# Optimization experiments

Measured on AMD Instinct MI355X. Metric: run time of the kernel, lower is better.

## Reference

```python
import jax, jax.numpy as jnp
import numpy as np

H = 2048          # hidden_size
HEAD = 64         # head_size
NH = H // HEAD    # n_heads = 32
B, T = 4, 4096
LORA_MIX = 32     # per-branch rank of time_maa low-rank mixer (5 branches)
LORA_DECAY = 64   # rank of decay low-rank mixer


def setup_inputs() -> dict:
    key = jax.random.key(0)
    ks = jax.random.split(key, 24)
    s = 0.02  # small init scale keeps tanh/silu in sane range
    inp = {
        "hidden": jax.random.normal(ks[0], (B, T, H), jnp.float32),
        "attn_x": jax.random.normal(ks[1], (B, H), jnp.float32),
        "attn_kv": jax.random.normal(ks[2], (B, NH, HEAD, HEAD), jnp.float32),
        "ffn_x": jax.random.normal(ks[3], (B, H), jnp.float32),
        "time_maa_x": jax.random.normal(ks[4], (1, 1, H), jnp.float32) * s,
        "time_maa_w": jax.random.normal(ks[5], (1, 1, H), jnp.float32) * s,
        "time_maa_k": jax.random.normal(ks[6], (1, 1, H), jnp.float32) * s,
        "time_maa_v": jax.random.normal(ks[7], (1, 1, H), jnp.float32) * s,
        "time_maa_r": jax.random.normal(ks[8], (1, 1, H), jnp.float32) * s,
        "time_maa_g": jax.random.normal(ks[9], (1, 1, H), jnp.float32) * s,
        "time_maa_w1": jax.random.normal(ks[10], (H, LORA_MIX * 5), jnp.float32) * s,
        "time_maa_w2": jax.random.normal(ks[11], (5, LORA_MIX, H), jnp.float32) * s,
        "time_decay": jax.random.normal(ks[12], (1, 1, H), jnp.float32) * s,
        "time_decay_w1": jax.random.normal(ks[13], (H, LORA_DECAY), jnp.float32) * s,
        "time_decay_w2": jax.random.normal(ks[14], (LORA_DECAY, H), jnp.float32) * s,
        "time_faaaa": jax.random.normal(ks[15], (NH, HEAD), jnp.float32) * s,
        "receptance_w": jax.random.normal(ks[16], (H, H), jnp.float32) * s,
        "key_w": jax.random.normal(ks[17], (H, H), jnp.float32) * s,
        "value_w": jax.random.normal(ks[18], (H, H), jnp.float32) * s,
        "gate_w": jax.random.normal(ks[19], (H, H), jnp.float32) * s,
        "output_w": jax.random.normal(ks[20], (H, H), jnp.float32) * s,
    }
    return inp


def reference(hidden, attn_x, attn_kv, ffn_x,
              time_maa_x, time_maa_w, time_maa_k, time_maa_v, time_maa_r, time_maa_g,
              time_maa_w1, time_maa_w2,
              time_decay, time_decay_w1, time_decay_w2, time_faaaa,
              receptance_w, key_w, value_w, gate_w, output_w):
    b, t, h = hidden.shape
    # token shift: prepend previous chunk's last token state
    shifted = jnp.concatenate([attn_x[:, None, :], hidden[:, :-1, :]], axis=1)  # [B,T,H]
    x = hidden
    xx = shifted - x
    # low-rank data-dependent mixing coefficients (5 branches)
    xxx = x + xx * time_maa_x                                        # [B,T,H]
    xxx = jnp.tanh(xxx.reshape(-1, h) @ time_maa_w1)                 # [B*T, 5*32]
    xxx = xxx.reshape(-1, 5, LORA_MIX).transpose(1, 0, 2)            # [5, B*T, 32]
    xxx = jnp.einsum('fnr,frh->fnh', xxx, time_maa_w2)               # [5, B*T, H]
    xxx = xxx.reshape(5, b, t, h)
    mw, mk, mv, mr, mg = xxx[0], xxx[1], xxx[2], xxx[3], xxx[4]
    # note: source uses additive mix (x + xx + coeff), faithful to code as written
    td_in = x + xx + (time_maa_w + mw)
    k_in = x + xx + (time_maa_k + mk)
    v_in = x + xx + (time_maa_v + mv)
    r_in = x + xx + (time_maa_r + mr)
    g_in = x + xx + (time_maa_g + mg)
    receptance = jnp.einsum('bth,hd->btd', r_in, receptance_w)
    key = jnp.einsum('bth,hd->btd', k_in, key_w)
    value = jnp.einsum('bth,hd->btd', v_in, value_w)
    gate = jax.nn.silu(jnp.einsum('bth,hd->btd', g_in, gate_w))
    td = jnp.tanh(jnp.einsum('bth,hr->btr', td_in, time_decay_w1))
    td = jnp.einsum('btr,rh->bth', td, time_decay_w2)
    td = time_decay + td                                              # [B,T,H] per-channel decay
    attn_x_new = hidden[:, -1]                                        # [B,H]
    return (receptance, key, value, gate, td, attn_x_new)
```

## Files before the change

kernel.cpp:

```cpp
#include <hip/hip_runtime.h>

#define H 2048
#define TT 4096
#define BB 4
#define NROWS (BB * TT)
#define NTH ((size_t)NROWS * H)
#define KCAT (H + 32)
#define KC8  (H + 64)
#define NTH64 ((size_t)NROWS * 64)

typedef __attribute__((ext_vector_type(8))) short bh8;
typedef __attribute__((ext_vector_type(4))) float f32x4;

__device__ inline unsigned short f2bf(float f) {
    union { float f; unsigned u; } v; v.f = f;
    unsigned r = v.u + 0x7fff + ((v.u >> 16) & 1);
    return (unsigned short)(r >> 16);
}
__device__ inline float bf2f(unsigned short u) {
    union { unsigned u; float f; } v; v.u = ((unsigned)u) << 16; return v.f;
}
__device__ inline void gload_lds16(const void* g, void* l) {
    __builtin_amdgcn_global_load_lds(
        (const __attribute__((address_space(1))) void*)g,
        (__attribute__((address_space(3))) void*)l, 16, 0, 0);
}

__global__ __launch_bounds__(256) void prep_kernel(
    const float* __restrict__ hidden, const float* __restrict__ attn_x,
    const float* __restrict__ tmx,
    unsigned short* __restrict__ shifted, unsigned short* __restrict__ xin) {
    size_t i = ((size_t)blockIdx.x * 256 + threadIdx.x) * 4;
    int n = (int)(i >> 11);
    int h = (int)(i & 2047);
    int t = n & (TT - 1);
    float4 x = *(const float4*)(hidden + i);
    float4 s;
    if (t == 0) {
        int b = n >> 12;
        s = *(const float4*)(attn_x + ((size_t)b << 11) + h);
    } else {
        s = *(const float4*)(hidden + (i - H));
    }
    float4 m = *(const float4*)(tmx + h);
    ushort4 sh, xi;
    sh.x = f2bf(s.x); sh.y = f2bf(s.y); sh.z = f2bf(s.z); sh.w = f2bf(s.w);
    xi.x = f2bf(x.x + (s.x - x.x) * m.x);
    xi.y = f2bf(x.y + (s.y - x.y) * m.y);
    xi.z = f2bf(x.z + (s.z - x.z) * m.z);
    xi.w = f2bf(x.w + (s.w - x.w) * m.w);
    *(ushort4*)(shifted + i) = sh;
    *(ushort4*)(xin + i) = xi;
}

__global__ __launch_bounds__(256) void transpose_kernel(
    const float* __restrict__ in, unsigned short* __restrict__ outp,
    int R, int C, int ldo) {
    __shared__ float tile[32][33];
    int tx = threadIdx.x & 31, ty = threadIdx.x >> 5;
    int r0 = blockIdx.y * 32, c0 = blockIdx.x * 32;
    for (int i = ty; i < 32; i += 8) {
        int r = r0 + i, c = c0 + tx;
        tile[i][tx] = (r < R && c < C) ? in[(size_t)r * C + c] : 0.f;
    }
    __syncthreads();
    for (int i = ty; i < 32; i += 8) {
        int c = c0 + i, r = r0 + tx;
        if (c < C && r < R) outp[(size_t)c * ldo + r] = f2bf(tile[tx][i]);
    }
}

__global__ __launch_bounds__(256) void transpose4_kernel(
    const float* __restrict__ w0, const float* __restrict__ w1,
    const float* __restrict__ w2, const float* __restrict__ w3,
    unsigned short* __restrict__ d0, unsigned short* __restrict__ d1,
    unsigned short* __restrict__ d2, unsigned short* __restrict__ d3) {
    __shared__ float tile[32][33];
    int bz = blockIdx.z;
    const float* in = bz == 0 ? w0 : bz == 1 ? w1 : bz == 2 ? w2 : w3;
    unsigned short* outp = bz == 0 ? d0 : bz == 1 ? d1 : bz == 2 ? d2 : d3;
    int tx = threadIdx.x & 31, ty = threadIdx.x >> 5;
    int r0 = blockIdx.y * 32, c0 = blockIdx.x * 32;
    for (int i = ty; i < 32; i += 8)
        tile[i][tx] = in[(size_t)(r0 + i) * H + c0 + tx];
    __syncthreads();
    for (int i = ty; i < 32; i += 8)
        outp[(size_t)(c0 + i) * KC8 + r0 + tx] = f2bf(tile[tx][i]);
}

__global__ __launch_bounds__(256) void w2wp_kernel(
    const float* __restrict__ W2,
    const float* __restrict__ w0, const float* __restrict__ w1,
    const float* __restrict__ w2, const float* __restrict__ w3,
    const float* __restrict__ W1d,
    float* __restrict__ part) {
    const int br = blockIdx.z, ks = blockIdx.y, dblk = blockIdx.x;
    const int tid = threadIdx.x;
    const float* W; int D;
    if (br < 4) { W = br == 0 ? w0 : br == 1 ? w1 : br == 2 ? w2 : w3; D = H; }
    else        { W = W1d; D = 64; }
    const int f = br < 4 ? ((0x4213 >> (br * 4)) & 15) : 0;
    const float* W2f = W2 + (size_t)f * 32 * H;
    __shared__ float w2s[256][32];
    const int k0 = ks * 256;
    for (int idx = tid; idx < 8192; idx += 256) {
        int r = idx & 31, kk = idx >> 5;
        w2s[kk][r] = W2f[(size_t)r * H + k0 + kk];
    }
    __syncthreads();
    int d = dblk * 256 + tid;
    if (d >= D) return;
    float a[32];
#pragma unroll
    for (int r = 0; r < 32; ++r) a[r] = 0.f;
    for (int kk = 0; kk < 256; ++kk) {
        float w = W[(size_t)(k0 + kk) * D + d];
        const float4* w4 = (const float4*)w2s[kk];
#pragma unroll
        for (int rq = 0; rq < 8; ++rq) {
            float4 v = w4[rq];
            a[rq * 4 + 0] += v.x * w;
            a[rq * 4 + 1] += v.y * w;
            a[rq * 4 + 2] += v.z * w;
            a[rq * 4 + 3] += v.w * w;
        }
    }
    float* pp = part + (((size_t)br * 8 + ks) * 32) * 2048 + d;
#pragma unroll
    for (int r = 0; r < 32; ++r) pp[(size_t)r * 2048] = a[r];
}

__global__ __launch_bounds__(256) void w2wr_kernel(
    const float* __restrict__ part,
    unsigned short* __restrict__ dR, unsigned short* __restrict__ dK,
    unsigned short* __restrict__ dV, unsigned short* __restrict__ dG,
    unsigned short* __restrict__ d1) {
    int gid = blockIdx.x * 256 + threadIdx.x;
    if (gid < 262144) {
        int br = gid >> 16, rem = gid & 65535;
        int r = rem >> 11, d = rem & 2047;
        float s = 0.f;
#pragma unroll
        for (int ks = 0; ks < 8; ++ks)
            s += part[(((size_t)br * 8 + ks) * 32 + r) * 2048 + d];
        unsigned short* dst = br == 0 ? dR : br == 1 ? dK : br == 2 ? dV : dG;
        dst[(size_t)d * KC8 + H + r] = f2bf(s);
        dst[(size_t)d * KC8 + H + 32 + r] = 0;
    } else {
        int q = gid - 262144;
        int r = q >> 6, d = q & 63;
        float s = 0.f;
#pragma unroll
        for (int ks = 0; ks < 8; ++ks)
            s += part[(((size_t)4 * 8 + ks) * 32 + r) * 2048 + d];
        d1[(size_t)d * KCAT + H + r] = f2bf(s);
    }
}

__global__ __launch_bounds__(256) void bias_all_kernel(
    const unsigned short* __restrict__ bR, const unsigned short* __restrict__ bK,
    const unsigned short* __restrict__ bV, const unsigned short* __restrict__ bG,
    const unsigned short* __restrict__ b1,
    const float* __restrict__ mR, const float* __restrict__ mK,
    const float* __restrict__ mV, const float* __restrict__ mG,
    const float* __restrict__ mW,
    float* __restrict__ bias4, float* __restrict__ bias0) {
    int wave = threadIdx.x >> 6, lane = threadIdx.x & 63;
    int p = blockIdx.x * 4 + wave;
    const unsigned short* src; const float* maa; float* dst;
    if (p < 8192) {
        int br = p >> 11, row = p & 2047;
        src = (br == 0 ? bR : br == 1 ? bK : br == 2 ? bV : bG) + (size_t)row * KC8;
        maa = (br == 0 ? mR : br == 1 ? mK : br == 2 ? mV : mG);
        dst = bias4 + br * H + row;
    } else {
        int q = p - 8192;
        if (q >= 64) return;
        src = b1 + (size_t)q * KCAT; maa = mW; dst = bias0 + q;
    }
    float a = 0.f;
#pragma unroll 4
    for (int i = 0; i < 32; ++i) { int h = i * 64 + lane; a += bf2f(src[h]) * maa[h]; }
    for (int s = 32; s; s >>= 1) a += __shfl_xor(a, s);
    if (lane == 0) *dst = a;
}

template <int WM, int WN, int FM, int FN, int HAS_BIAS, int ACT, int OF32, int ZPAD>
__global__ __launch_bounds__(256) void gemm_kernel(
    const unsigned short* __restrict__ A, int lda,
    const unsigned short* __restrict__ A2, int lda2, int KS,
    const unsigned short* __restrict__ Bt, int ldb, int K,
    void* __restrict__ outp, int ldo, int NT,
    const float* __restrict__ bias) {
    static_assert(WM * WN == 4, "4 waves");
    constexpr int BM = WM * FM * 16;
    constexpr int BN = WN * FN * 16;
    __shared__ unsigned short As[BM * 32];
    __shared__ unsigned short Bs[BN * 32];

    const int nb = gridDim.x;
    const int bid = blockIdx.x;
    const int swz = (bid & 7) * (nb >> 3) + (bid >> 3);
    const int mt = swz / NT, nt = swz % NT;
    const int m0 = mt * BM, n0 = nt * BN;

    const int tid = threadIdx.x;
    const int wave = tid >> 6, lane = tid & 63;
    const int l16 = lane & 15, kh = lane >> 4;
    const int wr = wave / WN, wc = wave % WN;

    f32x4 acc[FM][FN] = {};

    constexpr int ACH = BM * 4;
    constexpr int BCH = BN * 4;

    for (int k0 = 0; k0 < K; k0 += 32) {
#pragma unroll
        for (int i = 0; i < (ACH + 255) / 256; ++i) {
            int c = i * 256 + tid;
            if (ACH % 256 == 0 || c < ACH) {
                int row = c >> 2, ck = c & 3;
                int kk = k0 + ck * 8;
                const unsigned short* gp = (kk < KS)
                    ? A  + (size_t)(m0 + row) * lda  + kk
                    : A2 + (size_t)(m0 + row) * lda2 + (kk - KS);
                gload_lds16(gp, As + (size_t)(i * 256 + wave * 64) * 8);
            }
        }
#pragma unroll
        for (int i = 0; i < (BCH + 255) / 256; ++i) {
            int c = i * 256 + tid;
            if (BCH % 256 == 0 || c < BCH) {
                int row = c >> 2, ck = c & 3;
                gload_lds16(Bt + (size_t)(n0 + row) * ldb + k0 + ck * 8,
                            Bs + (size_t)(i * 256 + wave * 64) * 8);
            }
        }
        __syncthreads();
        bh8 av[FM], bv[FN];
#pragma unroll
        for (int mi = 0; mi < FM; ++mi)
            av[mi] = *(const bh8*)((const char*)As + (((wr * FM + mi) * 16 + l16) * 64 + kh * 16));
#pragma unroll
        for (int ni = 0; ni < FN; ++ni)
            bv[ni] = *(const bh8*)((const char*)Bs + (((wc * FN + ni) * 16 + l16) * 64 + kh * 16));
#pragma unroll
        for (int mi = 0; mi < FM; ++mi)
#pragma unroll
            for (int ni = 0; ni < FN; ++ni)
                acc[mi][ni] = __builtin_amdgcn_mfma_f32_16x16x32_bf16(
                    av[mi], bv[ni], acc[mi][ni], 0, 0, 0);
        __syncthreads();
    }

#pragma unroll
    for (int mi = 0; mi < FM; ++mi) {
#pragma unroll
        for (int ni = 0; ni < FN; ++ni) {
            int col = n0 + (wc * FN + ni) * 16 + l16;
            float bcol = HAS_BIAS ? bias[col] : 0.f;
#pragma unroll
            for (int j = 0; j < 4; ++j) {
                int row = m0 + (wr * FM + mi) * 16 + kh * 4 + j;
                float v = acc[mi][ni][j] + bcol;
                if (ACT == 1) v = v * (1.f / (1.f + __expf(-v)));
                else if (ACT == 2) v = tanhf(v);
                if (ZPAD) {
                    int br = col >> 5, cc = col & 31;
                    unsigned short* zp = (unsigned short*)outp
                        + (size_t)br * NTH64 + (size_t)row * 64 + cc;
                    zp[0] = f2bf(v);
                    zp[32] = 0;
                } else if (OF32) {
                    ((float*)outp)[(size_t)row * ldo + col] = v;
                } else {
                    ((unsigned short*)outp)[(size_t)row * ldo + col] = f2bf(v);
                }
            }
        }
    }
}

__global__ __launch_bounds__(512, 2) void bigproj8_kernel(
    const unsigned short* __restrict__ A,
    const unsigned short* __restrict__ zpad,
    const unsigned short* __restrict__ bt0, const unsigned short* __restrict__ bt1,
    const unsigned short* __restrict__ bt2, const unsigned short* __restrict__ bt3,
    const float* __restrict__ bias4, float* __restrict__ out) {
    constexpr int BUFB = 32768;
    constexpr int NTK = KC8 / 32;
    __shared__ alignas(16) char lds[4 * BUFB];

    const int bid = blockIdx.x;
    const int swz = (bid & 7) * 256 + (bid >> 3);
    const int branch = swz >> 9;
    const int tile = swz & 511;
    const int m0 = (tile >> 3) * 256, n0 = (tile & 7) * 256;

    const unsigned short* Bt = branch == 0 ? bt0 : branch == 1 ? bt1
                             : branch == 2 ? bt2 : bt3;
    const int f = (0x4213 >> (branch * 4)) & 15;
    const unsigned short* Az = zpad + (size_t)f * NTH64;

    const int tid = threadIdx.x;
    const int wave = tid >> 6, lane = tid & 63;
    const int l16 = lane & 15, kh = lane >> 4;
    const int wm = wave >> 2, wn = wave & 3;
    const int kh16 = kh * 16;
    const int swr = (l16 & 8) << 2;

    const int rS = tid >> 2;
    const int kbx = ((tid & 3) * 16) ^ ((rS & 8) << 2);
    const char* bA0 = (const char*)A  + (size_t)(m0 + rS) * 4096 + kbx;
    const char* bA1 = bA0 + (size_t)128 * 4096;
    const char* bz0 = (const char*)Az + (size_t)(m0 + rS) * 128 + kbx;
    const char* bz1 = bz0 + (size_t)128 * 128;
    const char* bB0 = (const char*)Bt + (size_t)(n0 + rS) * (KC8 * 2) + kbx;
    const char* bB1 = bB0 + (size_t)128 * (KC8 * 2);
    const int dA0 = wave * 1024, dA1 = 8192 + wave * 1024;

    auto stageA = [&](int kt, char* nb) {
        const char *p0, *p1;
        if (kt < 64) { size_t o = (size_t)kt * 64;        p0 = bA0 + o; p1 = bA1 + o; }
        else         { size_t o = (size_t)(kt - 64) * 64; p0 = bz0 + o; p1 = bz1 + o; }
        gload_lds16(p0, nb + dA0);
        gload_lds16(p1, nb + dA1);
    };
    auto stageB = [&](int kt, char* nb) {
        size_t o = (size_t)kt * 64;
        gload_lds16(bB0 + o, nb + 16384 + dA0);
        gload_lds16(bB1 + o, nb + 16384 + dA1);
    };

    f32x4 acc[8][4] = {};
    bh8 avlo[4], avhi[4], bvA[4], bvB[4];

    stageA(0, lds);        stageB(0, lds);
    stageA(1, lds + BUFB); stageB(1, lds + BUFB);
    asm volatile("s_waitcnt vmcnt(4)" ::: "memory");
    __builtin_amdgcn_s_barrier();
    __builtin_amdgcn_sched_barrier(0);
#pragma unroll
    for (int i = 0; i < 4; ++i) {
        avlo[i] = *(const bh8*)(lds + (wm * 8 + i) * 1024 + l16 * 64 + (kh16 ^ swr));
        bvA[i]  = *(const bh8*)(lds + 16384 + (wn * 4 + i) * 1024 + l16 * 64 + (kh16 ^ swr));
    }

    auto tile_step = [&](int t, bh8 (&bvC)[4], bh8 (&bvN)[4]) {
        const char* Ab = lds + (t & 3) * BUFB;
        char* nb = lds + ((t + 2) & 3) * BUFB;
        const bool doSt = (t + 2) < NTK;

#pragma unroll
        for (int i = 0; i < 4; ++i)
            avhi[i] = *(const bh8*)(Ab + (wm * 8 + 4 + i) * 1024 + l16 * 64 + (kh16 ^ swr));
        if (doSt) stageA(t + 2, nb);
        __builtin_amdgcn_s_setprio(1);
#pragma unroll
        for (int mi = 0; mi < 4; ++mi)
#pragma unroll
            for (int ni = 0; ni < 4; ++ni)
                acc[mi][ni] = __builtin_amdgcn_mfma_f32_16x16x32_bf16(
                    avlo[mi], bvC[ni], acc[mi][ni], 0, 0, 0);
        __builtin_amdgcn_s_setprio(0);

        if (doSt) stageB(t + 2, nb);
        if (t + 1 < NTK) {
            if (doSt) asm volatile("s_waitcnt vmcnt(4)" ::: "memory");
            else      asm volatile("s_waitcnt vmcnt(0)" ::: "memory");
            __builtin_amdgcn_s_barrier();
            __builtin_amdgcn_sched_barrier(0);
            const char* Ab1 = lds + ((t + 1) & 3) * BUFB;
#pragma unroll
            for (int i = 0; i < 4; ++i) {
                avlo[i] = *(const bh8*)(Ab1 + (wm * 8 + i) * 1024 + l16 * 64 + (kh16 ^ swr));
                bvN[i]  = *(const bh8*)(Ab1 + 16384 + (wn * 4 + i) * 1024 + l16 * 64 + (kh16 ^ swr));
            }
        }
        __builtin_amdgcn_s_setprio(1);
#pragma unroll
        for (int mi = 0; mi < 4; ++mi)
#pragma unroll
            for (int ni = 0; ni < 4; ++ni)
                acc[4 + mi][ni] = __builtin_amdgcn_mfma_f32_16x16x32_bf16(
                    avhi[mi], bvC[ni], acc[4 + mi][ni], 0, 0, 0);
        __builtin_amdgcn_s_setprio(0);
    };

    for (int t = 0; t < NTK; t += 2) {
        tile_step(t,     bvA, bvB);
        tile_step(t + 1, bvB, bvA);
    }

    float* outp = out + (size_t)branch * NTH;
    const float* bias = bias4 + branch * H;
#pragma unroll
    for (int a = 0; a < 8; ++a) {
#pragma unroll
        for (int b = 0; b < 4; ++b) {
            int col = n0 + wn * 64 + b * 16 + l16;
            float bc = bias[col];
#pragma unroll
            for (int j = 0; j < 4; ++j) {
                int row = m0 + wm * 128 + a * 16 + kh * 4 + j;
                float v = acc[a][b][j] + bc;
                if (branch == 3) v = v * (1.f / (1.f + __expf(-v)));
                outp[(size_t)row * H + col] = v;
            }
        }
    }
}

__global__ __launch_bounds__(256) void td2_kernel(
    const float* __restrict__ tdmid, const float* __restrict__ W2d,
    const float* __restrict__ tdecay, float* __restrict__ outp) {
    int col = blockIdx.x * 256 + threadIdx.x;
    int row0 = blockIdx.y * 8;
    float a[8] = {0, 0, 0, 0, 0, 0, 0, 0};
    for (int r = 0; r < 64; ++r) {
        float w = W2d[(size_t)r * H + col];
#pragma unroll
        for (int j = 0; j < 8; ++j)
            a[j] += tdmid[(size_t)(row0 + j) * 64 + r] * w;
    }
    float b = tdecay[col];
#pragma unroll
    for (int j = 0; j < 8; ++j)
        outp[(size_t)(row0 + j) * H + col] = a[j] + b;
}

__global__ __launch_bounds__(256) void axnew_kernel(
    const float* __restrict__ hidden, float* __restrict__ outp) {
    int i = blockIdx.x * 256 + threadIdx.x;
    int b = i >> 11, h = i & 2047;
    outp[i] = hidden[((size_t)(b * TT + (TT - 1)) << 11) + h];
}

extern "C" void kernel_launch(void* const* d_in, const int* in_sizes, int n_in,
                              void* d_out, int out_size, void* d_ws, size_t ws_size,
                              hipStream_t stream) {
    const float* hidden = (const float*)d_in[0];
    const float* attn_x = (const float*)d_in[1];
    const float* tmx    = (const float*)d_in[4];
    const float* tmaa_w = (const float*)d_in[5];
    const float* tmaa_k = (const float*)d_in[6];
    const float* tmaa_v = (const float*)d_in[7];
    const float* tmaa_r = (const float*)d_in[8];
    const float* tmaa_g = (const float*)d_in[9];
    const float* W1     = (const float*)d_in[10];
    const float* W2     = (const float*)d_in[11];
    const float* tdecay = (const float*)d_in[12];
    const float* W1d    = (const float*)d_in[13];
    const float* W2d    = (const float*)d_in[14];
    const float* Wr     = (const float*)d_in[16];
    const float* Wk     = (const float*)d_in[17];
    const float* Wv     = (const float*)d_in[18];
    const float* Wg     = (const float*)d_in[19];

    float* out = (float*)d_out;

    char* ws = (char*)d_ws;
    size_t off = 0;
    auto alloc = [&](size_t bytes) {
        char* p = ws + off;
        off = (off + bytes + 255) & ~(size_t)255;
        return p;
    };
    unsigned short* shifted = (unsigned short*)alloc(NTH * 2);
    unsigned short* xin     = (unsigned short*)alloc(NTH * 2);
    unsigned short* zpad    = (unsigned short*)alloc(5 * NTH64 * 2);
    unsigned short* W1t     = (unsigned short*)alloc((size_t)160 * H * 2);
    unsigned short* BcatR   = (unsigned short*)alloc((size_t)H * KC8 * 2);
    unsigned short* BcatK   = (unsigned short*)alloc((size_t)H * KC8 * 2);
    unsigned short* BcatV   = (unsigned short*)alloc((size_t)H * KC8 * 2);
    unsigned short* BcatG   = (unsigned short*)alloc((size_t)H * KC8 * 2);
    unsigned short* Bcat1   = (unsigned short*)alloc((size_t)64 * KCAT * 2);
    float* tdmid            = (float*)alloc((size_t)NROWS * 64 * 4);
    float* part             = (float*)alloc((size_t)5 * 8 * 32 * 2048 * 4);
    float* bias4            = (float*)alloc(4 * H * 4);
    float* bias0            = (float*)alloc(64 * 4);

    prep_kernel<<<(unsigned)(NTH / (4 * 256)), 256, 0, stream>>>(hidden, attn_x, tmx, shifted, xin);

    transpose4_kernel<<<dim3(64, 64, 4), 256, 0, stream>>>(
        Wr, Wk, Wv, Wg, BcatR, BcatK, BcatV, BcatG);
    transpose_kernel<<<dim3(5, 64), 256, 0, stream>>>(W1, W1t, H, 160, H);
    transpose_kernel<<<dim3(2, 64), 256, 0, stream>>>(W1d, Bcat1, H, 64, KCAT);
    w2wp_kernel<<<dim3(8, 8, 5), 256, 0, stream>>>(
        W2, Wr, Wk, Wv, Wg, W1d, part);
    w2wr_kernel<<<1032, 256, 0, stream>>>(
        part, BcatR, BcatK, BcatV, BcatG, Bcat1);
    bias_all_kernel<<<2064, 256, 0, stream>>>(
        BcatR, BcatK, BcatV, BcatG, Bcat1,
        tmaa_r, tmaa_k, tmaa_v, tmaa_g, tmaa_w, bias4, bias0);

    gemm_kernel<4, 1, 1, 10, 0, 2, 0, 1><<<256, 256, 0, stream>>>(
        xin, H, xin, H, H, W1t, H, H, zpad, 0, 1, nullptr);

    bigproj8_kernel<<<2048, 512, 0, stream>>>(
        shifted, zpad, BcatR, BcatK, BcatV, BcatG, bias4, out);

    gemm_kernel<4, 1, 1, 4, 1, 2, 1, 0><<<256, 256, 0, stream>>>(
        shifted, H, zpad, 64, H, Bcat1, KCAT, KCAT,
        tdmid, 64, 1, bias0);
    td2_kernel<<<dim3(8, NROWS / 8), 256, 0, stream>>>(
        tdmid, W2d, tdecay, out + 4 * NTH);

    axnew_kernel<<<32, 256, 0, stream>>>(hidden, out + 5 * NTH);
}
```

Baseline: 886.0 us.

## Restructure GEMM main loop into barrier-separated phases without register prefetch

Replaces the software-pipelined tile loop, which prefetched the next tile's A-low and B fragments into alternating register sets, with a simple per-tile loop. Each tile now loads its fragments, then runs two MFMA halves, and block-wide barriers with lgkmcnt waits sit around each half. The aim seems to be keeping waves in lockstep and cutting register pressure by dropping the double-buffered B fragments. In exchange, LDS read latency is no longer hidden behind MFMA work, and each tile adds extra barriers.

Measured after the change: 908.9 us. 2.6% more time.

```diff
diff --git a/kernel.cpp b/kernel.cpp
--- a/kernel.cpp
+++ b/kernel.cpp
@@ -333,63 +333,58 @@
     };
 
     f32x4 acc[8][4] = {};
-    bh8 avlo[4], avhi[4], bvA[4], bvB[4];
+    bh8 avlo[4], avhi[4], bv[4];
 
     stageA(0, lds);        stageB(0, lds);
     stageA(1, lds + BUFB); stageB(1, lds + BUFB);
     asm volatile("s_waitcnt vmcnt(4)" ::: "memory");
     __builtin_amdgcn_s_barrier();
     __builtin_amdgcn_sched_barrier(0);
-#pragma unroll
-    for (int i = 0; i < 4; ++i) {
-        avlo[i] = *(const bh8*)(lds + (wm * 8 + i) * 1024 + l16 * 64 + (kh16 ^ swr));
-        bvA[i]  = *(const bh8*)(lds + 16384 + (wn * 4 + i) * 1024 + l16 * 64 + (kh16 ^ swr));
-    }
-
-    auto tile_step = [&](int t, bh8 (&bvC)[4], bh8 (&bvN)[4]) {
-        const char* Ab = lds + (t & 3) * BUFB;
+
+    for (int t = 0; t < NTK; ++t) {
+        const char* cb = lds + (t & 3) * BUFB;
         char* nb = lds + ((t + 2) & 3) * BUFB;
         const bool doSt = (t + 2) < NTK;
 
 #pragma unroll
-        for (int i = 0; i < 4; ++i)
-            avhi[i] = *(const bh8*)(Ab + (wm * 8 + 4 + i) * 1024 + l16 * 64 + (kh16 ^ swr));
+        for (int i = 0; i < 4; ++i) {
+            avlo[i] = *(const bh8*)(cb + (wm * 8 + i) * 1024 + l16 * 64 + (kh16 ^ swr));
+            bv[i]   = *(const bh8*)(cb + 16384 + (wn * 4 + i) * 1024 + l16 * 64 + (kh16 ^ swr));
+        }
         if (doSt) stageA(t + 2, nb);
+        __builtin_amdgcn_s_barrier();
+        asm volatile("s_waitcnt lgkmcnt(0)" ::: "memory");
+        __builtin_amdgcn_sched_barrier(0);
         __builtin_amdgcn_s_setprio(1);
 #pragma unroll
         for (int mi = 0; mi < 4; ++mi)
 #pragma unroll
             for (int ni = 0; ni < 4; ++ni)
                 acc[mi][ni] = __builtin_amdgcn_mfma_f32_16x16x32_bf16(
-                    avlo[mi], bvC[ni], acc[mi][ni], 0, 0, 0);
+                    avlo[mi], bv[ni], acc[mi][ni], 0, 0, 0);
         __builtin_amdgcn_s_setprio(0);
-
+        __builtin_amdgcn_s_barrier();
+
+#pragma unroll
+        for (int i = 0; i < 4; ++i)
+            avhi[i] = *(const bh8*)(cb + (wm * 8 + 4 + i) * 1024 + l16 * 64 + (kh16 ^ swr));
         if (doSt) stageB(t + 2, nb);
         if (t + 1 < NTK) {
             if (doSt) asm volatile("s_waitcnt vmcnt(4)" ::: "memory");
             else      asm volatile("s_waitcnt vmcnt(0)" ::: "memory");
-            __builtin_amdgcn_s_barrier();
-            __builtin_amdgcn_sched_barrier(0);
-            const char* Ab1 = lds + ((t + 1) & 3) * BUFB;
-#pragma unroll
-            for (int i = 0; i < 4; ++i) {
-                avlo[i] = *(const bh8*)(Ab1 + (wm * 8 + i) * 1024 + l16 * 64 + (kh16 ^ swr));
-                bvN[i]  = *(const bh8*)(Ab1 + 16384 + (wn * 4 + i) * 1024 + l16 * 64 + (kh16 ^ swr));
-            }
-        }
+        }
+        __builtin_amdgcn_s_barrier();
+        asm volatile("s_waitcnt lgkmcnt(0)" ::: "memory");
+        __builtin_amdgcn_sched_barrier(0);
         __builtin_amdgcn_s_setprio(1);
 #pragma unroll
         for (int mi = 0; mi < 4; ++mi)
 #pragma unroll
             for (int ni = 0; ni < 4; ++ni)
                 acc[4 + mi][ni] = __builtin_amdgcn_mfma_f32_16x16x32_bf16(
-                    avhi[mi], bvC[ni], acc[4 + mi][ni], 0, 0, 0);
+                    avhi[mi], bv[ni], acc[4 + mi][ni], 0, 0, 0);
         __builtin_amdgcn_s_setprio(0);
-    };
-
-    for (int t = 0; t < NTK; t += 2) {
-        tile_step(t,     bvA, bvB);
-        tile_step(t + 1, bvB, bvA);
+        __builtin_amdgcn_s_barrier();
     }
 
     float* outp = out + (size_t)branch * NTH;
```
